# Kernel tuning notes

Hardware: AMD Instinct MI355X
Metric: run time of the kernel (lower is better)

Reference implementation:

```python
import jax, jax.numpy as jnp
import numpy as np

NUM_NODES = 2_000_000
INPUT_DIM = 128
NUM_GRAPHS = 16_384


def setup_inputs() -> dict:
    key = jax.random.key(0)
    k1, k2, k3 = jax.random.split(key, 3)
    x = jax.random.normal(k1, (NUM_NODES, INPUT_DIM), dtype=jnp.float32)
    batch = jnp.sort(jax.random.randint(k2, (NUM_NODES,), 0, NUM_GRAPHS, dtype=jnp.int64))
    # Linear(input_dim, 1) parameters
    W = jax.random.normal(k3, (INPUT_DIM, 1), dtype=jnp.float32) / np.sqrt(INPUT_DIM)
    b = jnp.zeros((1,), dtype=jnp.float32)
    return {"x": x, "batch": batch, "W": W, "b": b}


def reference(x, batch, W, b) -> jnp.ndarray:
    # scores: [N, 1]; softmax over dim=0 (ALL nodes, matching source exactly)
    scores = x @ W + b
    attn = jax.nn.softmax(scores, axis=0)  # [N, 1]
    # weighted features, then scatter-add by graph id (global_add_pool)
    pooled = jax.ops.segment_sum(x * attn, batch, num_segments=NUM_GRAPHS)
    return pooled  # [NUM_GRAPHS, INPUT_DIM]
```

## Files before the change

### kernel.cpp

```cpp
#include <hip/hip_runtime.h>
#include <math.h>

#define N_NODES  2000000
#define DIM      128
#define N_GRAPHS 16384

#define FBLOCKS  2048
#define WAVES    (FBLOCKS * 4)
#define RPW      ((N_NODES + WAVES - 1) / WAVES)

__global__ __launch_bounds__(256) void fused_kernel(const float* __restrict__ x,
                                                    const int* __restrict__ batch,
                                                    const float* __restrict__ W,
                                                    const float* __restrict__ b,
                                                    float* __restrict__ acc,
                                                    float* __restrict__ blkZ) {
    const int tid  = threadIdx.x;
    const int lane = tid & 63;
    const int l32  = lane & 31;
    const int half = lane >> 5;
    const int wave = blockIdx.x * 4 + (tid >> 6);

    const float4 wf  = ((const float4*)W)[l32];
    const float bias = b[0];

    const int r0 = wave * RPW;
    const int r1 = min(r0 + RPW, N_NODES);

    float zacc = 0.f;

    int r = r0;
    while (r < r1) {
        const int g = batch[r];
        int lo = r + 1, hi = r1;
        while (lo < hi) {
            const int mid = (lo + hi) >> 1;
            if (batch[mid] <= g) lo = mid + 1; else hi = mid;
        }
        const int end = lo;

        float4 racc = make_float4(0.f, 0.f, 0.f, 0.f);
        #pragma unroll 4
        for (int rr = r; rr < end; rr += 2) {
            const int row = rr + half;
            if (row < end) {
                const float4 xv = ((const float4*)(x + (long)row * DIM))[l32];
                float sv = xv.x * wf.x + xv.y * wf.y + xv.z * wf.z + xv.w * wf.w;
                #pragma unroll
                for (int m = 16; m >= 1; m >>= 1) sv += __shfl_xor(sv, m, 64);
                const float e = __expf(sv + bias);
                zacc += e;
                racc.x = fmaf(xv.x, e, racc.x);
                racc.y = fmaf(xv.y, e, racc.y);
                racc.z = fmaf(xv.z, e, racc.z);
                racc.w = fmaf(xv.w, e, racc.w);
            }
        }
        racc.x += __shfl_xor(racc.x, 32, 64);
        racc.y += __shfl_xor(racc.y, 32, 64);
        racc.z += __shfl_xor(racc.z, 32, 64);
        racc.w += __shfl_xor(racc.w, 32, 64);
        if (half == 0) {
            float* a = acc + (long)g * DIM + l32 * 4;
            atomicAdd(a + 0, racc.x);
            atomicAdd(a + 1, racc.y);
            atomicAdd(a + 2, racc.z);
            atomicAdd(a + 3, racc.w);
        }
        r = end;
    }

    zacc += __shfl_xor(zacc, 32, 64);
    __shared__ float sm[4];
    if (lane == 0) sm[tid >> 6] = zacc;
    __syncthreads();
    if (tid == 0) blkZ[blockIdx.x] = sm[0] + sm[1] + sm[2] + sm[3];
}

__global__ __launch_bounds__(256) void reduce_z_kernel(const float* __restrict__ blkZ,
                                                       float* __restrict__ invZ) {
    float v = 0.f;
    for (int i = threadIdx.x; i < FBLOCKS; i += 256) v += blkZ[i];
    __shared__ float sm[256];
    sm[threadIdx.x] = v;
    __syncthreads();
    #pragma unroll
    for (int st = 128; st >= 1; st >>= 1) {
        if (threadIdx.x < st) sm[threadIdx.x] += sm[threadIdx.x + st];
        __syncthreads();
    }
    if (threadIdx.x == 0) invZ[0] = 1.0f / sm[0];
}

__global__ __launch_bounds__(256) void finalize_kernel(const float* __restrict__ acc,
                                                       const float* __restrict__ invZ_ptr,
                                                       float* __restrict__ out) {
    const float invZ = invZ_ptr[0];
    const int i = blockIdx.x * 256 + threadIdx.x;
    const float4 v = ((const float4*)acc)[i];
    float4 o;
    o.x = v.x * invZ; o.y = v.y * invZ; o.z = v.z * invZ; o.w = v.w * invZ;
    ((float4*)out)[i] = o;
}

extern "C" void kernel_launch(void* const* d_in, const int* in_sizes, int n_in,
                              void* d_out, int out_size, void* d_ws, size_t ws_size,
                              hipStream_t stream) {
    const float* x     = (const float*)d_in[0];
    const int*   batch = (const int*)d_in[1];
    const float* W     = (const float*)d_in[2];
    const float* b     = (const float*)d_in[3];
    float* out = (float*)d_out;

    float* acc  = (float*)d_ws;
    float* blkZ = acc + (long)N_GRAPHS * DIM;
    float* invZ = blkZ + FBLOCKS;

    hipMemsetAsync(acc, 0, (size_t)N_GRAPHS * DIM * sizeof(float), stream);

    fused_kernel<<<FBLOCKS, 256, 0, stream>>>(x, batch, W, b, acc, blkZ);
    reduce_z_kernel<<<1, 256, 0, stream>>>(blkZ, invZ);

    const int fin_grid = (N_GRAPHS * DIM / 4) / 256;
    finalize_kernel<<<fin_grid, 256, 0, stream>>>(acc, invZ, out);
}
```

Measured before the change: 224.2 us.

## Process eight rows per wave iteration with transpose-style shuffle reduction; fold Z reduction into finalize

The main loop now loads four rows per half-wave and reduces the four dot products with a butterfly exchange that halves the number of cross-lane shuffles per row. The resulting exp weights are broadcast back with shuffles. The separate single-block Z reduction kernel is removed; every finalize block now re-reduces the per-block partial sums itself. The block count changes to 1792. The goals are more memory-level parallelism per wave, fewer shuffles, and one fewer kernel launch, at the cost of redundant Z reductions in the finalize blocks.

```diff
diff --git a/kernel.cpp b/kernel.cpp
--- a/kernel.cpp
+++ b/kernel.cpp
@@ -5,7 +5,7 @@
 #define DIM      128
 #define N_GRAPHS 16384
 
-#define FBLOCKS  2048
+#define FBLOCKS  1792
 #define WAVES    (FBLOCKS * 4)
 #define RPW      ((N_NODES + WAVES - 1) / WAVES)
 
@@ -27,7 +27,12 @@
     const int r0 = wave * RPW;
     const int r1 = min(r0 + RPW, N_NODES);
 
-    float zacc = 0.f;
+    float zb = 0.f;
+    float zt = 0.f;
+
+    const bool b4 = (l32 & 16) != 0;
+    const bool b3 = (l32 & 8) != 0;
+    const int ebase = lane & 32;
 
     int r = r0;
     while (r < r1) {
@@ -40,8 +45,60 @@
         const int end = lo;
 
         float4 racc = make_float4(0.f, 0.f, 0.f, 0.f);
-        #pragma unroll 4
-        for (int rr = r; rr < end; rr += 2) {
+
+        const int nb = (end - r) & ~7;
+        for (int rb = r; rb < r + nb; rb += 8) {
+            const float* bp = x + (long)(rb + half * 4) * DIM + l32 * 4;
+            const float4 xv0 = *(const float4*)(bp);
+            const float4 xv1 = *(const float4*)(bp + DIM);
+            const float4 xv2 = *(const float4*)(bp + 2 * DIM);
+            const float4 xv3 = *(const float4*)(bp + 3 * DIM);
+
+            float p0 = xv0.x * wf.x + xv0.y * wf.y + xv0.z * wf.z + xv0.w * wf.w;
+            float p1 = xv1.x * wf.x + xv1.y * wf.y + xv1.z * wf.z + xv1.w * wf.w;
+            float p2 = xv2.x * wf.x + xv2.y * wf.y + xv2.z * wf.z + xv2.w * wf.w;
+            float p3 = xv3.x * wf.x + xv3.y * wf.y + xv3.z * wf.z + xv3.w * wf.w;
+
+            float sA0 = b4 ? p0 : p2;
+            float sA1 = b4 ? p1 : p3;
+            float rA0 = __shfl_xor(sA0, 16, 64);
+            float rA1 = __shfl_xor(sA1, 16, 64);
+            float q0 = (b4 ? p2 : p0) + rA0;
+            float q1 = (b4 ? p3 : p1) + rA1;
+            float sB = b3 ? q0 : q1;
+            float rB = __shfl_xor(sB, 8, 64);
+            float s  = (b3 ? q1 : q0) + rB;
+            s += __shfl_xor(s, 4, 64);
+            s += __shfl_xor(s, 2, 64);
+            s += __shfl_xor(s, 1, 64);
+
+            const float e = __expf(s + bias);
+            zb += e;
+
+            const float e0 = __shfl(e, ebase + 0,  64);
+            const float e1 = __shfl(e, ebase + 8,  64);
+            const float e2 = __shfl(e, ebase + 16, 64);
+            const float e3 = __shfl(e, ebase + 24, 64);
+
+            racc.x = fmaf(xv0.x, e0, racc.x);
+            racc.y = fmaf(xv0.y, e0, racc.y);
+            racc.z = fmaf(xv0.z, e0, racc.z);
+            racc.w = fmaf(xv0.w, e0, racc.w);
+            racc.x = fmaf(xv1.x, e1, racc.x);
+            racc.y = fmaf(xv1.y, e1, racc.y);
+            racc.z = fmaf(xv1.z, e1, racc.z);
+            racc.w = fmaf(xv1.w, e1, racc.w);
+            racc.x = fmaf(xv2.x, e2, racc.x);
+            racc.y = fmaf(xv2.y, e2, racc.y);
+            racc.z = fmaf(xv2.z, e2, racc.z);
+            racc.w = fmaf(xv2.w, e2, racc.w);
+            racc.x = fmaf(xv3.x, e3, racc.x);
+            racc.y = fmaf(xv3.y, e3, racc.y);
+            racc.z = fmaf(xv3.z, e3, racc.z);
+            racc.w = fmaf(xv3.w, e3, racc.w);
+        }
+
+        for (int rr = r + nb; rr < end; rr += 2) {
             const int row = rr + half;
             if (row < end) {
                 const float4 xv = ((const float4*)(x + (long)row * DIM))[l32];
@@ -49,13 +106,14 @@
                 #pragma unroll
                 for (int m = 16; m >= 1; m >>= 1) sv += __shfl_xor(sv, m, 64);
                 const float e = __expf(sv + bias);
-                zacc += e;
+                zt += e;
                 racc.x = fmaf(xv.x, e, racc.x);
                 racc.y = fmaf(xv.y, e, racc.y);
                 racc.z = fmaf(xv.z, e, racc.z);
                 racc.w = fmaf(xv.w, e, racc.w);
             }
         }
+
         racc.x += __shfl_xor(racc.x, 32, 64);
         racc.y += __shfl_xor(racc.y, 32, 64);
         racc.z += __shfl_xor(racc.z, 32, 64);
@@ -70,18 +128,23 @@
         r = end;
     }
 
-    zacc += __shfl_xor(zacc, 32, 64);
+    float z = zb * 0.125f + zt * 0.03125f;
+    #pragma unroll
+    for (int m = 32; m >= 1; m >>= 1) z += __shfl_xor(z, m, 64);
+
     __shared__ float sm[4];
-    if (lane == 0) sm[tid >> 6] = zacc;
+    if (lane == 0) sm[tid >> 6] = z;
     __syncthreads();
     if (tid == 0) blkZ[blockIdx.x] = sm[0] + sm[1] + sm[2] + sm[3];
 }
 
-__global__ __launch_bounds__(256) void reduce_z_kernel(const float* __restrict__ blkZ,
-                                                       float* __restrict__ invZ) {
+__global__ __launch_bounds__(256) void finalize_kernel(const float* __restrict__ acc,
+                                                       const float* __restrict__ blkZ,
+                                                       float* __restrict__ out) {
+    __shared__ float sm[256];
     float v = 0.f;
-    for (int i = threadIdx.x; i < FBLOCKS; i += 256) v += blkZ[i];
-    __shared__ float sm[256];
+    #pragma unroll
+    for (int i = 0; i < FBLOCKS / 256; ++i) v += blkZ[i * 256 + threadIdx.x];
     sm[threadIdx.x] = v;
     __syncthreads();
     #pragma unroll
@@ -89,17 +152,12 @@
         if (threadIdx.x < st) sm[threadIdx.x] += sm[threadIdx.x + st];
         __syncthreads();
     }
-    if (threadIdx.x == 0) invZ[0] = 1.0f / sm[0];
-}
+    const float invZ = 1.0f / sm[0];
 
-__global__ __launch_bounds__(256) void finalize_kernel(const float* __restrict__ acc,
-                                                       const float* __restrict__ invZ_ptr,
-                                                       float* __restrict__ out) {
-    const float invZ = invZ_ptr[0];
     const int i = blockIdx.x * 256 + threadIdx.x;
-    const float4 v = ((const float4*)acc)[i];
+    const float4 a = ((const float4*)acc)[i];
     float4 o;
-    o.x = v.x * invZ; o.y = v.y * invZ; o.z = v.z * invZ; o.w = v.w * invZ;
+    o.x = a.x * invZ; o.y = a.y * invZ; o.z = a.z * invZ; o.w = a.w * invZ;
     ((float4*)out)[i] = o;
 }
 
@@ -114,13 +172,11 @@
 
     float* acc  = (float*)d_ws;
     float* blkZ = acc + (long)N_GRAPHS * DIM;
-    float* invZ = blkZ + FBLOCKS;
 
     hipMemsetAsync(acc, 0, (size_t)N_GRAPHS * DIM * sizeof(float), stream);
 
     fused_kernel<<<FBLOCKS, 256, 0, stream>>>(x, batch, W, b, acc, blkZ);
-    reduce_z_kernel<<<1, 256, 0, stream>>>(blkZ, invZ);
 
     const int fin_grid = (N_GRAPHS * DIM / 4) / 256;
-    finalize_kernel<<<fin_grid, 256, 0, stream>>>(acc, invZ, out);
+    finalize_kernel<<<fin_grid, 256, 0, stream>>>(acc, blkZ, out);
 }
```

New measurement: 238.7 us. 1.06x slower.
